# Kernel tuning notes

Hardware: AMD Instinct MI355X
Metric: run time of the kernel (lower is better)

Reference implementation:

```python
import jax, jax.numpy as jnp
import numpy as np

N = 50000
E = 400000
H1, H2, D = 4, 2, 64
NEG_SLOPE = 0.2
EPS = 1e-5


def _segment_softmax(alpha, dst, num_nodes):
    # alpha: [E, H], softmax over edges sharing the same dst node
    m = jax.ops.segment_max(alpha, dst, num_segments=num_nodes)  # [N, H]
    ex = jnp.exp(alpha - m[dst])
    den = jax.ops.segment_sum(ex, dst, num_segments=num_nodes)   # [N, H]
    return ex / den[dst]


def _gat_conv(x, src, dst, eattr, W, We, a_src, a_dst, a_edge, b, heads, num_nodes):
    # x: [N, Fin] -> h: [N, H, D]; eattr: [E, Fe] -> e: [E, H, D]
    h = (x @ W).reshape(num_nodes, heads, D)
    e = (eattr @ We).reshape(-1, heads, D)
    al_src = jnp.einsum('nhd,hd->nh', h, a_src)   # [N, H]
    al_dst = jnp.einsum('nhd,hd->nh', h, a_dst)   # [N, H]
    al_e = jnp.einsum('ehd,hd->eh', e, a_edge)    # [E, H]
    alpha = al_src[src] + al_dst[dst] + al_e
    alpha = jax.nn.leaky_relu(alpha, NEG_SLOPE)
    alpha = _segment_softmax(alpha, dst, num_nodes)
    msg = h[src] * alpha[:, :, None]              # [E, H, D]
    out = jax.ops.segment_sum(msg, dst, num_segments=num_nodes)
    return out.reshape(num_nodes, heads * D) + b


def _graph_norm(x, w, b, mean_scale):
    # PyG GraphNorm over the whole (single) graph
    mean = jnp.mean(x, axis=0, keepdims=True)
    out = x - mean * mean_scale
    var = jnp.mean(out * out, axis=0, keepdims=True)
    return w * out / jnp.sqrt(var + EPS) + b


def _forward(x, edge_index, edge_attr,
             W1, We1, as1, ad1, ae1, b1, gn1_w, gn1_b, gn1_ms,
             W2, We2, as2, ad2, ae2, b2, gn2_w, gn2_b, gn2_ms,
             Wc, bc):
    # add self loops (PyG default), self-loop edge_attr = mean of edge_attr
    loops = jnp.arange(N)
    src = jnp.concatenate([edge_index[0], loops])
    dst = jnp.concatenate([edge_index[1], loops])
    ea_mean = jnp.mean(edge_attr, axis=0, keepdims=True)
    eattr = jnp.concatenate([edge_attr, jnp.broadcast_to(ea_mean, (N, edge_attr.shape[1]))])

    h = _gat_conv(x, src, dst, eattr, W1, We1, as1, ad1, ae1, b1, H1, N)
    h = jax.nn.elu(_graph_norm(h, gn1_w, gn1_b, gn1_ms))
    h = _gat_conv(h, src, dst, eattr, W2, We2, as2, ad2, ae2, b2, H2, N)
    h = jax.nn.elu(_graph_norm(h, gn2_w, gn2_b, gn2_ms))
    return h @ Wc + bc


def setup_inputs() -> dict:
    key = jax.random.key(0)
    ks = jax.random.split(key, 20)
    g = lambda k, shape, fan: jax.random.normal(k, shape, jnp.float32) * (1.0 / np.sqrt(fan))
    inp = {
        'x': jax.random.normal(ks[0], (N, 3), jnp.float32),
        'edge_index': jax.random.randint(ks[1], (2, E), 0, N),
        'edge_attr': jax.random.uniform(ks[2], (E, 2), jnp.float32),
        'W1': g(ks[3], (3, H1 * D), 3),
        'We1': g(ks[4], (2, H1 * D), 2),
        'as1': g(ks[5], (H1, D), D),
        'ad1': g(ks[6], (H1, D), D),
        'ae1': g(ks[7], (H1, D), D),
        'b1': jnp.zeros((H1 * D,), jnp.float32),
        'gn1_w': jnp.ones((H1 * D,), jnp.float32),
        'gn1_b': jnp.zeros((H1 * D,), jnp.float32),
        'gn1_ms': jnp.ones((H1 * D,), jnp.float32),
        'W2': g(ks[8], (H1 * D, H2 * D), H1 * D),
        'We2': g(ks[9], (2, H2 * D), 2),
        'as2': g(ks[10], (H2, D), D),
        'ad2': g(ks[11], (H2, D), D),
        'ae2': g(ks[12], (H2, D), D),
        'b2': jnp.zeros((H2 * D,), jnp.float32),
        'gn2_w': jnp.ones((H2 * D,), jnp.float32),
        'gn2_b': jnp.zeros((H2 * D,), jnp.float32),
        'gn2_ms': jnp.ones((H2 * D,), jnp.float32),
        # classifier 128 -> 13
        'Wc': g(ks[13], (H2 * D, 13), H2 * D),
        'bc': jnp.zeros((13,), jnp.float32),
    }
    return inp


def reference(x, edge_index, edge_attr,
              W1, We1, as1, ad1, ae1, b1, gn1_w, gn1_b, gn1_ms,
              W2, We2, as2, ad2, ae2, b2, gn2_w, gn2_b, gn2_ms,
              Wc, bc):
    return _forward(x, edge_index, edge_attr,
                    W1, We1, as1, ad1, ae1, b1, gn1_w, gn1_b, gn1_ms,
                    W2, We2, as2, ad2, ae2, b2, gn2_w, gn2_b, gn2_ms,
                    Wc, bc)
```

## Files before the change

### kernel.cpp

```cpp
#include <hip/hip_runtime.h>
#include <math.h>

#define NEG_SLOPE 0.2f
#define GEPS 1e-5f

typedef __attribute__((ext_vector_type(8))) short short8;
typedef __attribute__((ext_vector_type(4))) float floatx4;

__device__ __forceinline__ float wave_reduce_sum(float v) {
#pragma unroll
    for (int o = 32; o > 0; o >>= 1) v += __shfl_down(v, o);
    return v;
}

__device__ __forceinline__ ushort f2bf(float f) {
    union { float f; unsigned int i; } c;
    c.f = f;
    unsigned int b = c.i;
    b += 0x7fffu + ((b >> 16) & 1u);
    return (ushort)(b >> 16);
}

__device__ __forceinline__ float bf2f(ushort u) {
    union { unsigned int i; float f; } c;
    c.i = (unsigned int)u << 16;
    return c.f;
}

__device__ __forceinline__ float2 unpack_bf2(unsigned int u) {
    union { unsigned int i; float f; } a, b;
    a.i = u << 16;
    b.i = u & 0xffff0000u;
    return make_float2(a.f, b.f);
}

__device__ __forceinline__ unsigned int pack_bf2(float lo, float hi) {
    return (unsigned int)f2bf(lo) | ((unsigned int)f2bf(hi) << 16);
}

__device__ __forceinline__ float lrelu(float v) {
    return (v > 0.f) ? v : v * NEG_SLOPE;
}

__device__ __forceinline__ float elu_fast(float v) {
    return (v > 0.f) ? v : (__expf(v) - 1.f);
}

__global__ __launch_bounds__(256) void k_pre(
    const float* __restrict__ x, const float* __restrict__ W1,
    const float* __restrict__ as1, const float* __restrict__ ad1,
    const float* __restrict__ ea, const int* __restrict__ dst,
    const float* __restrict__ W2, const float* __restrict__ We1,
    const float* __restrict__ ae1, const float* __restrict__ We2,
    const float* __restrict__ ae2,
    ushort* __restrict__ h1, float* __restrict__ al_s, float* __restrict__ al_d,
    float* __restrict__ ea_sum, int* __restrict__ deg, uint4* __restrict__ Bfrag,
    float* __restrict__ C1, float* __restrict__ C2, int N, int E, int NB1) {
    int b = blockIdx.x;
    if (b < NB1) {
        int u = threadIdx.x >> 7;
        int n = b * 2 + u;
        if (n >= N) return;
        int t = threadIdx.x & 127, lane = threadIdx.x & 63;
        int c0 = 2 * t;
        float x0 = x[3 * n], x1 = x[3 * n + 1], x2 = x[3 * n + 2];
        float h0 = fmaf(x0, W1[c0], fmaf(x1, W1[256 + c0], x2 * W1[512 + c0]));
        float h1v = fmaf(x0, W1[c0 + 1], fmaf(x1, W1[257 + c0], x2 * W1[513 + c0]));
        ((unsigned int*)h1)[(size_t)n * 128 + t] = pack_bf2(h0, h1v);
        float ps = h0 * as1[c0] + h1v * as1[c0 + 1];
        float pd = h0 * ad1[c0] + h1v * ad1[c0 + 1];
#pragma unroll
        for (int o = 16; o > 0; o >>= 1) {
            ps += __shfl_xor(ps, o);
            pd += __shfl_xor(pd, o);
        }
        if ((lane & 31) == 0) {
            int h = c0 >> 6;
            al_s[n * 4 + h] = ps;
            al_d[n * 4 + h] = pd;
        }
        return;
    }
    b -= NB1;
    if (b < 16) {
        int t = b * 256 + threadIdx.x;
        int c = t >> 9, kk = (t >> 6) & 7, L = t & 63;
        int q = L >> 4, n = c * 16 + (L & 15);
        int k0 = kk * 32 + q * 8;
        unsigned int u0 = pack_bf2(W2[(k0 + 0) * 128 + n], W2[(k0 + 1) * 128 + n]);
        unsigned int u1 = pack_bf2(W2[(k0 + 2) * 128 + n], W2[(k0 + 3) * 128 + n]);
        unsigned int u2 = pack_bf2(W2[(k0 + 4) * 128 + n], W2[(k0 + 5) * 128 + n]);
        unsigned int u3 = pack_bf2(W2[(k0 + 6) * 128 + n], W2[(k0 + 7) * 128 + n]);
        Bfrag[t] = make_uint4(u0, u1, u2, u3);
        return;
    }
    if (b == 16) {
        int t = threadIdx.x, h = t >> 6, lane = t & 63;
        float p0 = We1[t] * ae1[t];
        float p1 = We1[256 + t] * ae1[t];
        p0 = wave_reduce_sum(p0);
        p1 = wave_reduce_sum(p1);
        if (lane == 0) { C1[h] = p0; C1[4 + h] = p1; }
        if (t < 128) {
            float q0 = We2[t] * ae2[t];
            float q1 = We2[128 + t] * ae2[t];
            q0 = wave_reduce_sum(q0);
            q1 = wave_reduce_sum(q1);
            if (lane == 0) { C2[h] = q0; C2[2 + h] = q1; }
        }
        return;
    }
    b -= 17;
    const float2* ea2 = (const float2*)ea;
    float s0 = 0.f, s1 = 0.f;
    for (int e = b * 256 + threadIdx.x; e < E; e += 256 * 256) {
        float2 v = ea2[e];
        s0 += v.x; s1 += v.y;
        atomicAdd(&deg[dst[e]], 1);
    }
    s0 = wave_reduce_sum(s0);
    s1 = wave_reduce_sum(s1);
    if ((threadIdx.x & 63) == 0) {
        atomicAdd(&ea_sum[0], s0);
        atomicAdd(&ea_sum[1], s1);
    }
}

__global__ void k_scan1(const int* __restrict__ deg, int* __restrict__ row_ptr,
                        int* __restrict__ bsum, int N) {
    __shared__ int tmp[1024];
    int tid = threadIdx.x;
    int i = blockIdx.x * 1024 + tid;
    int v = (i < N) ? deg[i] : 0;
    tmp[tid] = v;
    __syncthreads();
#pragma unroll
    for (int off = 1; off < 1024; off <<= 1) {
        int t = (tid >= off) ? tmp[tid - off] : 0;
        __syncthreads();
        tmp[tid] += t;
        __syncthreads();
    }
    if (i < N) row_ptr[i + 1] = tmp[tid];
    if (tid == 1023) bsum[blockIdx.x] = tmp[1023];
}

__global__ void k_scan23(int* __restrict__ row_ptr, const int* __restrict__ bsum,
                         const float* __restrict__ ea_sum, const float* __restrict__ C1,
                         const float* __restrict__ C2, float* __restrict__ lE1,
                         float* __restrict__ lE2, int N, int E) {
    __shared__ int off_s;
    int t = threadIdx.x;
    if (blockIdx.x == 0 && t >= 64 && t < 68) {
        int k = t - 64;
        float m0 = ea_sum[0] / (float)E, m1 = ea_sum[1] / (float)E;
        lE1[k] = m0 * C1[k] + m1 * C1[4 + k];
        if (k < 2) lE2[k] = m0 * C2[k] + m1 * C2[2 + k];
    }
    if (t < 64) {
        int v = (t < blockIdx.x) ? bsum[t] : 0;
#pragma unroll
        for (int o = 32; o > 0; o >>= 1) v += __shfl_xor(v, o);
        if (t == 0) off_s = v;
    }
    __syncthreads();
    int off = off_s;
    int i = blockIdx.x * 1024 + t;
    if (i == 0) row_ptr[0] = 0;
    if (i < N) row_ptr[i + 1] += off;
}

__global__ void k_scatfill(const int* __restrict__ dst, const int* __restrict__ src,
                           const float* __restrict__ ea, const int* __restrict__ row_ptr,
                           int* __restrict__ deg, const float* __restrict__ al_s1,
                           const float* __restrict__ al_d1, const float* __restrict__ C1,
                           float4* __restrict__ ed2, uint4* __restrict__ wmp, int E) {
    int e = blockIdx.x * 256 + threadIdx.x;
    if (e >= E) return;
    int d = dst[e];
    int r = atomicSub(&deg[d], 1);
    int slot = row_ptr[d] + r - 1;
    int s = src[e];
    float2 v = ((const float2*)ea)[e];
    float4 as = *(const float4*)(al_s1 + 4 * (size_t)s);
    float4 ad = *(const float4*)(al_d1 + 4 * (size_t)d);
    float w0 = __expf(lrelu(as.x + ad.x + v.x * C1[0] + v.y * C1[4]));
    float w1 = __expf(lrelu(as.y + ad.y + v.x * C1[1] + v.y * C1[5]));
    float w2 = __expf(lrelu(as.z + ad.z + v.x * C1[2] + v.y * C1[6]));
    float w3 = __expf(lrelu(as.w + ad.w + v.x * C1[3] + v.y * C1[7]));
    ed2[slot] = make_float4(__int_as_float(s), __int_as_float(d), v.x, v.y);
    wmp[slot] = make_uint4((unsigned int)s, pack_bf2(w0, w1), pack_bf2(w2, w3), 0u);
}

__global__ void k_fill2(const float4* __restrict__ ed2, const float* __restrict__ al_s2,
                        const float* __restrict__ al_d2, const float* __restrict__ C2,
                        float4* __restrict__ wm2, int E) {
    int e = blockIdx.x * 256 + threadIdx.x;
    if (e >= E) return;
    float4 m = ed2[e];
    int s = __float_as_int(m.x), d = __float_as_int(m.y);
    float2 as = *(const float2*)(al_s2 + 2 * (size_t)s);
    float2 ad = *(const float2*)(al_d2 + 2 * (size_t)d);
    float wA = __expf(lrelu(as.x + ad.x + m.z * C2[0] + m.w * C2[2]));
    float wB = __expf(lrelu(as.y + ad.y + m.z * C2[1] + m.w * C2[3]));
    wm2[e] = make_float4(m.x, wA, wB, 0.f);
}

__global__ __launch_bounds__(256) void k_agg1(const ushort* __restrict__ h1,
                                              const int* __restrict__ row_ptr,
                                              const uint4* __restrict__ wmp,
                                              const float* __restrict__ al_s,
                                              const float* __restrict__ al_d,
                                              const float* __restrict__ lE,
                                              const float* __restrict__ bias,
                                              ushort* __restrict__ out, int N) {
    int n = blockIdx.x * 4 + (threadIdx.x >> 6);
    if (n >= N) return;
    int lane = threadIdx.x & 63;
    int g = lane >> 5, c32 = lane & 31;
    int h = c32 >> 3;
    const uint4* h1u4 = (const uint4*)h1;
    float4 as = *(const float4*)(al_s + 4 * (size_t)n);
    float4 ad = *(const float4*)(al_d + 4 * (size_t)n);
    float4 le = *(const float4*)lE;
    float ws0 = __expf(lrelu(as.x + ad.x + le.x));
    float ws1 = __expf(lrelu(as.y + ad.y + le.y));
    float ws2 = __expf(lrelu(as.z + ad.z + le.z));
    float ws3 = __expf(lrelu(as.w + ad.w + le.w));
    float wsh = (h == 0) ? ws0 : (h == 1) ? ws1 : (h == 2) ? ws2 : ws3;
    uint4 hs = h1u4[(size_t)n * 32 + c32];
    float wself = (g == 0) ? wsh : 0.f;
    float dsum = wself;
    float acc[8];
    {
        float2 t0 = unpack_bf2(hs.x), t1 = unpack_bf2(hs.y);
        float2 t2 = unpack_bf2(hs.z), t3 = unpack_bf2(hs.w);
        acc[0] = wself * t0.x; acc[1] = wself * t0.y;
        acc[2] = wself * t1.x; acc[3] = wself * t1.y;
        acc[4] = wself * t2.x; acc[5] = wself * t2.y;
        acc[6] = wself * t3.x; acc[7] = wself * t3.y;
    }
    int i0 = row_ptr[n];
    int cnt = row_ptr[n + 1] - i0;
    if (cnt > 0) {
        int last = cnt - 1;
        int nit = (cnt + 1) >> 1;
        int j0 = g;     float mkA = 1.f; if (j0 > last) { j0 = last; mkA = 0.f; }
        int j1 = 2 + g; float mkB = 1.f; if (j1 > last) { j1 = last; mkB = 0.f; }
        int j2 = 4 + g; float mkC = 1.f; if (j2 > last) { j2 = last; mkC = 0.f; }
        int j3 = 6 + g; float mkD = 1.f; if (j3 > last) { j3 = last; mkD = 0.f; }
        uint4 meA = wmp[i0 + j0];
        uint4 meB = wmp[i0 + j1];
        uint4 meC = wmp[i0 + j2];
        uint4 meD = wmp[i0 + j3];
        uint4 gvA = h1u4[(size_t)meA.x * 32 + c32];
        uint4 gvB = h1u4[(size_t)meB.x * 32 + c32];
        uint4 gvC = h1u4[(size_t)meC.x * 32 + c32];
        for (int it = 0; it < nit - 1; ++it) {
            uint4 gvD = h1u4[(size_t)meD.x * 32 + c32];
            int jn = 2 * (it + 4) + g;
            float mn = 1.f;
            if (jn > last) { jn = last; mn = 0.f; }
            uint4 meE = wmp[i0 + jn];
            float2 w01 = unpack_bf2(meA.y);
            float2 w23 = unpack_bf2(meA.z);
            float2 wp = (h < 2) ? w01 : w23;
            float wg = ((h & 1) ? wp.y : wp.x) * mkA;
            dsum += wg;
            float2 u;
            u = unpack_bf2(gvA.x); acc[0] = fmaf(wg, u.x, acc[0]); acc[1] = fmaf(wg, u.y, acc[1]);
            u = unpack_bf2(gvA.y); acc[2] = fmaf(wg, u.x, acc[2]); acc[3] = fmaf(wg, u.y, acc[3]);
            u = unpack_bf2(gvA.z); acc[4] = fmaf(wg, u.x, acc[4]); acc[5] = fmaf(wg, u.y, acc[5]);
            u = unpack_bf2(gvA.w); acc[6] = fmaf(wg, u.x, acc[6]); acc[7] = fmaf(wg, u.y, acc[7]);
            meA = meB; meB = meC; meC = meD; meD = meE;
            gvA = gvB; gvB = gvC; gvC = gvD;
            mkA = mkB; mkB = mkC; mkC = mkD; mkD = mn;
        }
        float2 w01 = unpack_bf2(meA.y);
        float2 w23 = unpack_bf2(meA.z);
        float2 wp = (h < 2) ? w01 : w23;
        float wg = ((h & 1) ? wp.y : wp.x) * mkA;
        dsum += wg;
        float2 u;
        u = unpack_bf2(gvA.x); acc[0] = fmaf(wg, u.x, acc[0]); acc[1] = fmaf(wg, u.y, acc[1]);
        u = unpack_bf2(gvA.y); acc[2] = fmaf(wg, u.x, acc[2]); acc[3] = fmaf(wg, u.y, acc[3]);
        u = unpack_bf2(gvA.z); acc[4] = fmaf(wg, u.x, acc[4]); acc[5] = fmaf(wg, u.y, acc[5]);
        u = unpack_bf2(gvA.w); acc[6] = fmaf(wg, u.x, acc[6]); acc[7] = fmaf(wg, u.y, acc[7]);
    }
#pragma unroll
    for (int k = 0; k < 8; ++k) acc[k] += __shfl_xor(acc[k], 32);
    dsum += __shfl_xor(dsum, 32);
    if (g == 0) {
        float inv = 1.f / dsum;
        const float* bp = bias + c32 * 8;
        float4 b0 = *(const float4*)bp;
        float4 b1 = *(const float4*)(bp + 4);
        uint4 o;
        o.x = pack_bf2(fmaf(acc[0], inv, b0.x), fmaf(acc[1], inv, b0.y));
        o.y = pack_bf2(fmaf(acc[2], inv, b0.z), fmaf(acc[3], inv, b0.w));
        o.z = pack_bf2(fmaf(acc[4], inv, b1.x), fmaf(acc[5], inv, b1.y));
        o.w = pack_bf2(fmaf(acc[6], inv, b1.z), fmaf(acc[7], inv, b1.w));
        ((uint4*)out)[(size_t)n * 32 + c32] = o;
    }
}

__global__ __launch_bounds__(256) void k_agg2(const ushort* __restrict__ h2,
                                              const int* __restrict__ row_ptr,
                                              const float4* __restrict__ wm,
                                              const float* __restrict__ al_s,
                                              const float* __restrict__ al_d,
                                              const float* __restrict__ lE,
                                              const float* __restrict__ bias,
                                              ushort* __restrict__ out, int N) {
    int n = blockIdx.x * 4 + (threadIdx.x >> 6);
    if (n >= N) return;
    int lane = threadIdx.x & 63;
    int g = lane >> 4, c16 = lane & 15;
    bool hi = c16 >= 8;
    const uint4* h2u4 = (const uint4*)h2;
    float2 ad = *(const float2*)(al_d + 2 * (size_t)n);
    float2 as = *(const float2*)(al_s + 2 * (size_t)n);
    float wsA = __expf(lrelu(as.x + ad.x + lE[0]));
    float wsB = __expf(lrelu(as.y + ad.y + lE[1]));
    uint4 hs = h2u4[(size_t)n * 16 + c16];
    float wself = (g == 0) ? (hi ? wsB : wsA) : 0.f;
    float dsum = wself;
    float acc[8];
    {
        float2 t0 = unpack_bf2(hs.x), t1 = unpack_bf2(hs.y);
        float2 t2 = unpack_bf2(hs.z), t3 = unpack_bf2(hs.w);
        acc[0] = wself * t0.x; acc[1] = wself * t0.y;
        acc[2] = wself * t1.x; acc[3] = wself * t1.y;
        acc[4] = wself * t2.x; acc[5] = wself * t2.y;
        acc[6] = wself * t3.x; acc[7] = wself * t3.y;
    }
    int i0 = row_ptr[n];
    int cnt = row_ptr[n + 1] - i0;
    if (cnt > 0) {
        int last = cnt - 1;
        int nit = (cnt + 3) >> 2;
        int j0 = g;      float mkA = 1.f; if (j0 > last) { j0 = last; mkA = 0.f; }
        int j1 = 4 + g;  float mkB = 1.f; if (j1 > last) { j1 = last; mkB = 0.f; }
        int j2 = 8 + g;  float mkC = 1.f; if (j2 > last) { j2 = last; mkC = 0.f; }
        int j3 = 12 + g; float mkD = 1.f; if (j3 > last) { j3 = last; mkD = 0.f; }
        float4 meA = wm[i0 + j0];
        float4 meB = wm[i0 + j1];
        float4 meC = wm[i0 + j2];
        float4 meD = wm[i0 + j3];
        uint4 gvA = h2u4[(size_t)__float_as_int(meA.x) * 16 + c16];
        uint4 gvB = h2u4[(size_t)__float_as_int(meB.x) * 16 + c16];
        uint4 gvC = h2u4[(size_t)__float_as_int(meC.x) * 16 + c16];
        for (int it = 0; it < nit - 1; ++it) {
            uint4 gvD = h2u4[(size_t)__float_as_int(meD.x) * 16 + c16];
            int jn = 4 * (it + 4) + g;
            float mn = 1.f;
            if (jn > last) { jn = last; mn = 0.f; }
            float4 meE = wm[i0 + jn];
            float wg = (hi ? meA.z : meA.y) * mkA;
            dsum += wg;
            float2 u;
            u = unpack_bf2(gvA.x); acc[0] = fmaf(wg, u.x, acc[0]); acc[1] = fmaf(wg, u.y, acc[1]);
            u = unpack_bf2(gvA.y); acc[2] = fmaf(wg, u.x, acc[2]); acc[3] = fmaf(wg, u.y, acc[3]);
            u = unpack_bf2(gvA.z); acc[4] = fmaf(wg, u.x, acc[4]); acc[5] = fmaf(wg, u.y, acc[5]);
            u = unpack_bf2(gvA.w); acc[6] = fmaf(wg, u.x, acc[6]); acc[7] = fmaf(wg, u.y, acc[7]);
            meA = meB; meB = meC; meC = meD; meD = meE;
            gvA = gvB; gvB = gvC; gvC = gvD;
            mkA = mkB; mkB = mkC; mkC = mkD; mkD = mn;
        }
        float wg = (hi ? meA.z : meA.y) * mkA;
        dsum += wg;
        float2 u;
        u = unpack_bf2(gvA.x); acc[0] = fmaf(wg, u.x, acc[0]); acc[1] = fmaf(wg, u.y, acc[1]);
        u = unpack_bf2(gvA.y); acc[2] = fmaf(wg, u.x, acc[2]); acc[3] = fmaf(wg, u.y, acc[3]);
        u = unpack_bf2(gvA.z); acc[4] = fmaf(wg, u.x, acc[4]); acc[5] = fmaf(wg, u.y, acc[5]);
        u = unpack_bf2(gvA.w); acc[6] = fmaf(wg, u.x, acc[6]); acc[7] = fmaf(wg, u.y, acc[7]);
    }
#pragma unroll
    for (int k = 0; k < 8; ++k) {
        acc[k] += __shfl_xor(acc[k], 16);
        acc[k] += __shfl_xor(acc[k], 32);
    }
    dsum += __shfl_xor(dsum, 16);
    dsum += __shfl_xor(dsum, 32);
    if (g == 0) {
        float inv = 1.f / dsum;
        const float* bp = bias + c16 * 8;
        float4 b0 = *(const float4*)bp;
        float4 b1 = *(const float4*)(bp + 4);
        uint4 o;
        o.x = pack_bf2(fmaf(acc[0], inv, b0.x), fmaf(acc[1], inv, b0.y));
        o.y = pack_bf2(fmaf(acc[2], inv, b0.z), fmaf(acc[3], inv, b0.w));
        o.z = pack_bf2(fmaf(acc[4], inv, b1.x), fmaf(acc[5], inv, b1.y));
        o.w = pack_bf2(fmaf(acc[6], inv, b1.z), fmaf(acc[7], inv, b1.w));
        ((uint4*)out)[(size_t)n * 16 + c16] = o;
    }
}

template <int C4>
__global__ __launch_bounds__(256) void k_stats_bf(const ushort* __restrict__ x,
                                                  float* __restrict__ stats, int rows) {
    const int C = C4 * 8;
    const int RG = 256 / C4;
    int t = threadIdx.x;
    int c = t & (C4 - 1);
    int rg = t / C4;
    int rpb = (rows + gridDim.x - 1) / gridDim.x;
    int r0 = blockIdx.x * rpb;
    int r1 = r0 + rpb;
    if (r1 > rows) r1 = rows;
    const uint4* xu = (const uint4*)x;
    float s[8] = {0.f, 0.f, 0.f, 0.f, 0.f, 0.f, 0.f, 0.f};
    float q[8] = {0.f, 0.f, 0.f, 0.f, 0.f, 0.f, 0.f, 0.f};
    for (int r = r0 + rg; r < r1; r += RG) {
        uint4 v = xu[(size_t)r * C4 + c];
        float2 a0 = unpack_bf2(v.x), a1 = unpack_bf2(v.y);
        float2 a2 = unpack_bf2(v.z), a3 = unpack_bf2(v.w);
        s[0] += a0.x; q[0] = fmaf(a0.x, a0.x, q[0]);
        s[1] += a0.y; q[1] = fmaf(a0.y, a0.y, q[1]);
        s[2] += a1.x; q[2] = fmaf(a1.x, a1.x, q[2]);
        s[3] += a1.y; q[3] = fmaf(a1.y, a1.y, q[3]);
        s[4] += a2.x; q[4] = fmaf(a2.x, a2.x, q[4]);
        s[5] += a2.y; q[5] = fmaf(a2.y, a2.y, q[5]);
        s[6] += a3.x; q[6] = fmaf(a3.x, a3.x, q[6]);
        s[7] += a3.y; q[7] = fmaf(a3.y, a3.y, q[7]);
    }
    __shared__ float ls[256 * 16];
#pragma unroll
    for (int k = 0; k < 8; ++k) {
        ls[t * 16 + k] = s[k];
        ls[t * 16 + 8 + k] = q[k];
    }
    __syncthreads();
    if (t < C) {
        int cc = t >> 3, k = t & 7;
        float ssum = 0.f, qsum = 0.f;
#pragma unroll
        for (int g = 0; g < RG; ++g) {
            ssum += ls[(g * C4 + cc) * 16 + k];
            qsum += ls[(g * C4 + cc) * 16 + 8 + k];
        }
        atomicAdd(&stats[t], ssum);
        atomicAdd(&stats[C + t], qsum);
    }
}

__global__ __launch_bounds__(256) void k_gemm2_mfma(const ushort* __restrict__ X,
                                                    const float* __restrict__ stats,
                                                    const float* __restrict__ gw,
                                                    const float* __restrict__ gb,
                                                    const float* __restrict__ gms,
                                                    const uint4* __restrict__ Bfrag,
                                                    const float* __restrict__ as2,
                                                    const float* __restrict__ ad2,
                                                    ushort* __restrict__ H2,
                                                    float* __restrict__ al_s,
                                                    float* __restrict__ al_d, int Nn) {
    __shared__ __align__(16) float ABs[512];
    {
        int t = threadIdx.x;
        float inv = 1.f / (float)Nn;
        float mean = stats[t] * inv;
        float cm = mean * gms[t];
        float var = stats[256 + t] * inv - 2.f * cm * mean + cm * cm;
        float A = gw[t] * rsqrtf(var + GEPS);
        ABs[t] = A;
        ABs[256 + t] = gb[t] - A * cm;
    }
    __syncthreads();
    int wave = threadIdx.x >> 6, lane = threadIdx.x & 63;
    int q = lane >> 4, m = lane & 15;
    int rowbase = blockIdx.x * 64 + wave * 16;
    int row = rowbase + m;
    bool valid = row < Nn;
    const uint4* xr4 = (const uint4*)((const unsigned int*)X + (size_t)row * 128);
    uint4 xa[8];
// ... 163 lines not shown
    const float* We2 = (const float*)d_in[13];
    const float* as2 = (const float*)d_in[14];
    const float* ad2 = (const float*)d_in[15];
    const float* ae2 = (const float*)d_in[16];
    const float* b2 = (const float*)d_in[17];
    const float* gn2_w = (const float*)d_in[18];
    const float* gn2_b = (const float*)d_in[19];
    const float* gn2_ms = (const float*)d_in[20];
    const float* Wc = (const float*)d_in[21];
    const float* bc = (const float*)d_in[22];

    const int N = in_sizes[0] / 3;
    const int E = in_sizes[1] / 2;
    const int* srcv = edge_index;
    const int* dstv = edge_index + E;

    char* w = (char*)d_ws;
    auto carveB = [&](size_t bytes) -> void* {
        void* p = (void*)w;
        w += ((bytes + 255) / 256) * 256;
        return p;
    };
    int* deg = (int*)carveB((size_t)N * 4);
    float* ea_sum = (float*)carveB(8);
    float* statsA = (float*)carveB(512 * 4);
    float* statsB = (float*)carveB(256 * 4);
    char* zero_end = w;
    int* row_ptr = (int*)carveB((size_t)(N + 1) * 4);
    int* bsum = (int*)carveB(1024 * 4);
    float4* ed2 = (float4*)carveB((size_t)E * 16);
    uint4* wmp = (uint4*)carveB((size_t)E * 16);
    float4* wm2 = (float4*)wmp;
    float* C1 = (float*)carveB(8 * 4);
    float* lE1 = (float*)carveB(4 * 4);
    float* C2 = (float*)carveB(4 * 4);
    float* lE2 = (float*)carveB(2 * 4);
    uint4* Bfrag = (uint4*)carveB(4096 * 16);
    float* al_s1 = (float*)carveB((size_t)N * 4 * 4);
    float* al_d1 = (float*)carveB((size_t)N * 4 * 4);
    float* al_s2 = (float*)carveB((size_t)N * 2 * 4);
    float* al_d2 = (float*)carveB((size_t)N * 2 * 4);
    ushort* h1b = (ushort*)carveB((size_t)N * 256 * 2);
    ushort* h2b = (ushort*)carveB((size_t)N * 128 * 2);
    ushort* out1b = (ushort*)carveB((size_t)N * 256 * 2);
    ushort* out2b = h1b;

    hipMemsetAsync(deg, 0, (size_t)(zero_end - (char*)deg), stream);

    const int nb1 = (N + 1023) / 1024;
    const int ebl = (E + 255) / 256;
    const int NB1 = (N + 1) / 2;

    k_pre<<<NB1 + 17 + 256, 256, 0, stream>>>(x, W1, as1, ad1, edge_attr, dstv, W2, We1, ae1,
                                              We2, ae2, h1b, al_s1, al_d1, ea_sum, deg, Bfrag,
                                              C1, C2, N, E, NB1);
    k_scan1<<<nb1, 1024, 0, stream>>>(deg, row_ptr, bsum, N);
    k_scan23<<<nb1, 1024, 0, stream>>>(row_ptr, bsum, ea_sum, C1, C2, lE1, lE2, N, E);
    k_scatfill<<<ebl, 256, 0, stream>>>(dstv, srcv, edge_attr, row_ptr, deg, al_s1, al_d1, C1,
                                        ed2, wmp, E);
    k_agg1<<<(N + 3) / 4, 256, 0, stream>>>(h1b, row_ptr, wmp, al_s1, al_d1, lE1, b1, out1b, N);
    k_stats_bf<32><<<256, 256, 0, stream>>>(out1b, statsA, N);
    k_gemm2_mfma<<<(N + 63) / 64, 256, 0, stream>>>(out1b, statsA, gn1_w, gn1_b, gn1_ms, Bfrag,
                                                    as2, ad2, h2b, al_s2, al_d2, N);
    k_fill2<<<ebl, 256, 0, stream>>>(ed2, al_s2, al_d2, C2, wm2, E);
    k_agg2<<<(N + 3) / 4, 256, 0, stream>>>(h2b, row_ptr, wm2, al_s2, al_d2, lE2, b2, out2b, N);
    k_stats_bf<16><<<256, 256, 0, stream>>>(out2b, statsB, N);
    k_cls<<<(N + 15) / 16, 256, 0, stream>>>(out2b, statsB, gn2_w, gn2_b, gn2_ms, Wc, bc,
                                             (float*)d_out, N);
}
```

Measured before the change: 320.9 us.

## Aggregate raw 3-dim inputs before projecting, fuse GraphNorm stats into aggregation

Layer-1 aggregation now uses linearity: it gathers the 3-float source features, accumulates a per-head weighted sum (12 values), and applies W1 after normalisation. This removes the materialised 256-wide bf16 h1 and its heavy per-edge gathers. Attention logits for layer 1 are computed from precomputed W1·a projections inside the scan kernel. Both aggregation kernels become grid-stride and accumulate GraphNorm column sums and squares in place, with block-level atomics replacing the separate stats kernels. The cost is extra shuffle reductions per node and a fixed block count.

```diff
diff --git a/kernel.cpp b/kernel.cpp
--- a/kernel.cpp
+++ b/kernel.cpp
@@ -3,6 +3,8 @@
 
 #define NEG_SLOPE 0.2f
 #define GEPS 1e-5f
+#define AGG1_BLOCKS 2048
+#define AGG2_BLOCKS 2048
 
 typedef __attribute__((ext_vector_type(8))) short short8;
 typedef __attribute__((ext_vector_type(4))) float floatx4;
@@ -47,41 +49,15 @@
 }
 
 __global__ __launch_bounds__(256) void k_pre(
-    const float* __restrict__ x, const float* __restrict__ W1,
-    const float* __restrict__ as1, const float* __restrict__ ad1,
+    const float* __restrict__ W1, const float* __restrict__ as1, const float* __restrict__ ad1,
     const float* __restrict__ ea, const int* __restrict__ dst,
     const float* __restrict__ W2, const float* __restrict__ We1,
     const float* __restrict__ ae1, const float* __restrict__ We2,
     const float* __restrict__ ae2,
-    ushort* __restrict__ h1, float* __restrict__ al_s, float* __restrict__ al_d,
     float* __restrict__ ea_sum, int* __restrict__ deg, uint4* __restrict__ Bfrag,
-    float* __restrict__ C1, float* __restrict__ C2, int N, int E, int NB1) {
+    float* __restrict__ C1, float* __restrict__ C2, float* __restrict__ Ps,
+    float* __restrict__ Pd, int E) {
     int b = blockIdx.x;
-    if (b < NB1) {
-        int u = threadIdx.x >> 7;
-        int n = b * 2 + u;
-        if (n >= N) return;
-        int t = threadIdx.x & 127, lane = threadIdx.x & 63;
-        int c0 = 2 * t;
-        float x0 = x[3 * n], x1 = x[3 * n + 1], x2 = x[3 * n + 2];
-        float h0 = fmaf(x0, W1[c0], fmaf(x1, W1[256 + c0], x2 * W1[512 + c0]));
-        float h1v = fmaf(x0, W1[c0 + 1], fmaf(x1, W1[257 + c0], x2 * W1[513 + c0]));
-        ((unsigned int*)h1)[(size_t)n * 128 + t] = pack_bf2(h0, h1v);
-        float ps = h0 * as1[c0] + h1v * as1[c0 + 1];
-        float pd = h0 * ad1[c0] + h1v * ad1[c0 + 1];
-#pragma unroll
-        for (int o = 16; o > 0; o >>= 1) {
-            ps += __shfl_xor(ps, o);
-            pd += __shfl_xor(pd, o);
-        }
-        if ((lane & 31) == 0) {
-            int h = c0 >> 6;
-            al_s[n * 4 + h] = ps;
-            al_d[n * 4 + h] = pd;
-        }
-        return;
-    }
-    b -= NB1;
     if (b < 16) {
         int t = b * 256 + threadIdx.x;
         int c = t >> 9, kk = (t >> 6) & 7, L = t & 63;
@@ -101,6 +77,14 @@
         p0 = wave_reduce_sum(p0);
         p1 = wave_reduce_sum(p1);
         if (lane == 0) { C1[h] = p0; C1[4 + h] = p1; }
+        float av = as1[t], dv = ad1[t];
+#pragma unroll
+        for (int k = 0; k < 3; ++k) {
+            float wv = W1[k * 256 + t];
+            float ps = wave_reduce_sum(wv * av);
+            float pd = wave_reduce_sum(wv * dv);
+            if (lane == 0) { Ps[h * 3 + k] = ps; Pd[h * 3 + k] = pd; }
+        }
         if (t < 128) {
             float q0 = We2[t] * ae2[t];
             float q1 = We2[128 + t] * ae2[t];
@@ -147,8 +131,10 @@
 
 __global__ void k_scan23(int* __restrict__ row_ptr, const int* __restrict__ bsum,
                          const float* __restrict__ ea_sum, const float* __restrict__ C1,
-                         const float* __restrict__ C2, float* __restrict__ lE1,
-                         float* __restrict__ lE2, int N, int E) {
+                         const float* __restrict__ C2, const float* __restrict__ Ps,
+                         const float* __restrict__ Pd, const float* __restrict__ x,
+                         float* __restrict__ al_s1, float* __restrict__ al_d1,
+                         float* __restrict__ lE1, float* __restrict__ lE2, int N, int E) {
     __shared__ int off_s;
     int t = threadIdx.x;
     if (blockIdx.x == 0 && t >= 64 && t < 68) {
@@ -167,7 +153,21 @@
     int off = off_s;
     int i = blockIdx.x * 1024 + t;
     if (i == 0) row_ptr[0] = 0;
-    if (i < N) row_ptr[i + 1] += off;
+    if (i < N) {
+        row_ptr[i + 1] += off;
+        float x0 = x[3 * i], x1 = x[3 * i + 1], x2 = x[3 * i + 2];
+        float4 sv, dv;
+        sv.x = fmaf(x0, Ps[0], fmaf(x1, Ps[1], x2 * Ps[2]));
+        sv.y = fmaf(x0, Ps[3], fmaf(x1, Ps[4], x2 * Ps[5]));
+        sv.z = fmaf(x0, Ps[6], fmaf(x1, Ps[7], x2 * Ps[8]));
+        sv.w = fmaf(x0, Ps[9], fmaf(x1, Ps[10], x2 * Ps[11]));
+        dv.x = fmaf(x0, Pd[0], fmaf(x1, Pd[1], x2 * Pd[2]));
+        dv.y = fmaf(x0, Pd[3], fmaf(x1, Pd[4], x2 * Pd[5]));
+        dv.z = fmaf(x0, Pd[6], fmaf(x1, Pd[7], x2 * Pd[8]));
+        dv.w = fmaf(x0, Pd[9], fmaf(x1, Pd[10], x2 * Pd[11]));
+        *(float4*)(al_s1 + 4 * (size_t)i) = sv;
+        *(float4*)(al_d1 + 4 * (size_t)i) = dv;
+    }
 }
 
 __global__ void k_scatfill(const int* __restrict__ dst, const int* __restrict__ src,
@@ -206,101 +206,121 @@
     wm2[e] = make_float4(m.x, wA, wB, 0.f);
 }
 
-__global__ __launch_bounds__(256) void k_agg1(const ushort* __restrict__ h1,
+__global__ __launch_bounds__(256) void k_agg1(const float* __restrict__ x,
                                               const int* __restrict__ row_ptr,
                                               const uint4* __restrict__ wmp,
                                               const float* __restrict__ al_s,
                                               const float* __restrict__ al_d,
                                               const float* __restrict__ lE,
+                                              const float* __restrict__ W1,
                                               const float* __restrict__ bias,
-                                              ushort* __restrict__ out, int N) {
-    int n = blockIdx.x * 4 + (threadIdx.x >> 6);
-    if (n >= N) return;
-    int lane = threadIdx.x & 63;
-    int g = lane >> 5, c32 = lane & 31;
-    int h = c32 >> 3;
-    const uint4* h1u4 = (const uint4*)h1;
-    float4 as = *(const float4*)(al_s + 4 * (size_t)n);
-    float4 ad = *(const float4*)(al_d + 4 * (size_t)n);
-    float4 le = *(const float4*)lE;
-    float ws0 = __expf(lrelu(as.x + ad.x + le.x));
-    float ws1 = __expf(lrelu(as.y + ad.y + le.y));
-    float ws2 = __expf(lrelu(as.z + ad.z + le.z));
-    float ws3 = __expf(lrelu(as.w + ad.w + le.w));
-    float wsh = (h == 0) ? ws0 : (h == 1) ? ws1 : (h == 2) ? ws2 : ws3;
-    uint4 hs = h1u4[(size_t)n * 32 + c32];
-    float wself = (g == 0) ? wsh : 0.f;
-    float dsum = wself;
-    float acc[8];
+                                              ushort* __restrict__ out,
+                                              float* __restrict__ stats, int N) {
+    int l = threadIdx.x & 31;
+    int grp = threadIdx.x >> 5;
+    int c0 = l * 8;
+    int hh = l >> 3;
+    float4 wa0 = *(const float4*)(W1 + c0);
+    float4 wa1 = *(const float4*)(W1 + c0 + 4);
+    float4 wb0 = *(const float4*)(W1 + 256 + c0);
+    float4 wb1 = *(const float4*)(W1 + 256 + c0 + 4);
+    float4 wc0 = *(const float4*)(W1 + 512 + c0);
+    float4 wc1 = *(const float4*)(W1 + 512 + c0 + 4);
+    float4 bv0 = *(const float4*)(bias + c0);
+    float4 bv1 = *(const float4*)(bias + c0 + 4);
+    float le0 = lE[0], le1 = lE[1], le2 = lE[2], le3 = lE[3];
+    float s8[8] = {0.f, 0.f, 0.f, 0.f, 0.f, 0.f, 0.f, 0.f};
+    float q8[8] = {0.f, 0.f, 0.f, 0.f, 0.f, 0.f, 0.f, 0.f};
+    for (int n = blockIdx.x * 8 + grp; n < N; n += AGG1_BLOCKS * 8) {
+        float4 asn = *(const float4*)(al_s + 4 * (size_t)n);
+        float4 adn = *(const float4*)(al_d + 4 * (size_t)n);
+        float ws0 = __expf(lrelu(asn.x + adn.x + le0));
+        float ws1 = __expf(lrelu(asn.y + adn.y + le1));
+        float ws2 = __expf(lrelu(asn.z + adn.z + le2));
+        float ws3 = __expf(lrelu(asn.w + adn.w + le3));
+        float z[12];
+        float ds[4];
+#pragma unroll
+        for (int k = 0; k < 12; ++k) z[k] = 0.f;
+#pragma unroll
+        for (int k = 0; k < 4; ++k) ds[k] = 0.f;
+        int i0 = row_ptr[n];
+        int cnt = row_ptr[n + 1] - i0;
+        for (int j = l; j < cnt; j += 32) {
+            uint4 me = wmp[i0 + j];
+            int s = (int)me.x;
+            float xs0 = x[3 * s], xs1 = x[3 * s + 1], xs2 = x[3 * s + 2];
+            float2 w01 = unpack_bf2(me.y);
+            float2 w23 = unpack_bf2(me.z);
+            z[0] = fmaf(w01.x, xs0, z[0]); z[1] = fmaf(w01.x, xs1, z[1]); z[2] = fmaf(w01.x, xs2, z[2]);
+            z[3] = fmaf(w01.y, xs0, z[3]); z[4] = fmaf(w01.y, xs1, z[4]); z[5] = fmaf(w01.y, xs2, z[5]);
+            z[6] = fmaf(w23.x, xs0, z[6]); z[7] = fmaf(w23.x, xs1, z[7]); z[8] = fmaf(w23.x, xs2, z[8]);
+            z[9] = fmaf(w23.y, xs0, z[9]); z[10] = fmaf(w23.y, xs1, z[10]); z[11] = fmaf(w23.y, xs2, z[11]);
+            ds[0] += w01.x; ds[1] += w01.y; ds[2] += w23.x; ds[3] += w23.y;
+        }
+#pragma unroll
+        for (int o = 16; o > 0; o >>= 1) {
+#pragma unroll
+            for (int k = 0; k < 12; ++k) z[k] += __shfl_xor(z[k], o);
+#pragma unroll
+            for (int k = 0; k < 4; ++k) ds[k] += __shfl_xor(ds[k], o);
+        }
+        float xn0 = x[3 * n], xn1 = x[3 * n + 1], xn2 = x[3 * n + 2];
+        z[0] = fmaf(ws0, xn0, z[0]); z[1] = fmaf(ws0, xn1, z[1]); z[2] = fmaf(ws0, xn2, z[2]);
+        z[3] = fmaf(ws1, xn0, z[3]); z[4] = fmaf(ws1, xn1, z[4]); z[5] = fmaf(ws1, xn2, z[5]);
+        z[6] = fmaf(ws2, xn0, z[6]); z[7] = fmaf(ws2, xn1, z[7]); z[8] = fmaf(ws2, xn2, z[8]);
+        z[9] = fmaf(ws3, xn0, z[9]); z[10] = fmaf(ws3, xn1, z[10]); z[11] = fmaf(ws3, xn2, z[11]);
+        ds[0] += ws0; ds[1] += ws1; ds[2] += ws2; ds[3] += ws3;
+        float zh0 = (hh == 0) ? z[0] : (hh == 1) ? z[3] : (hh == 2) ? z[6] : z[9];
+        float zh1 = (hh == 0) ? z[1] : (hh == 1) ? z[4] : (hh == 2) ? z[7] : z[10];
+        float zh2 = (hh == 0) ? z[2] : (hh == 1) ? z[5] : (hh == 2) ? z[8] : z[11];
+        float dsh = (hh == 0) ? ds[0] : (hh == 1) ? ds[1] : (hh == 2) ? ds[2] : ds[3];
+        float inv = 1.f / dsh;
+        float v0 = fmaf(fmaf(zh0, wa0.x, fmaf(zh1, wb0.x, zh2 * wc0.x)), inv, bv0.x);
+        float v1 = fmaf(fmaf(zh0, wa0.y, fmaf(zh1, wb0.y, zh2 * wc0.y)), inv, bv0.y);
+        float v2 = fmaf(fmaf(zh0, wa0.z, fmaf(zh1, wb0.z, zh2 * wc0.z)), inv, bv0.z);
+        float v3 = fmaf(fmaf(zh0, wa0.w, fmaf(zh1, wb0.w, zh2 * wc0.w)), inv, bv0.w);
+        float v4 = fmaf(fmaf(zh0, wa1.x, fmaf(zh1, wb1.x, zh2 * wc1.x)), inv, bv1.x);
+        float v5 = fmaf(fmaf(zh0, wa1.y, fmaf(zh1, wb1.y, zh2 * wc1.y)), inv, bv1.y);
+        float v6 = fmaf(fmaf(zh0, wa1.z, fmaf(zh1, wb1.z, zh2 * wc1.z)), inv, bv1.z);
+        float v7 = fmaf(fmaf(zh0, wa1.w, fmaf(zh1, wb1.w, zh2 * wc1.w)), inv, bv1.w);
+        ushort u0 = f2bf(v0), u1 = f2bf(v1), u2 = f2bf(v2), u3 = f2bf(v3);
+        ushort u4 = f2bf(v4), u5 = f2bf(v5), u6 = f2bf(v6), u7 = f2bf(v7);
+        float r0 = bf2f(u0), r1 = bf2f(u1), r2 = bf2f(u2), r3 = bf2f(u3);
+        float r4 = bf2f(u4), r5 = bf2f(u5), r6 = bf2f(u6), r7 = bf2f(u7);
+        s8[0] += r0; q8[0] = fmaf(r0, r0, q8[0]);
+        s8[1] += r1; q8[1] = fmaf(r1, r1, q8[1]);
+        s8[2] += r2; q8[2] = fmaf(r2, r2, q8[2]);
+        s8[3] += r3; q8[3] = fmaf(r3, r3, q8[3]);
+        s8[4] += r4; q8[4] = fmaf(r4, r4, q8[4]);
+        s8[5] += r5; q8[5] = fmaf(r5, r5, q8[5]);
+        s8[6] += r6; q8[6] = fmaf(r6, r6, q8[6]);
+        s8[7] += r7; q8[7] = fmaf(r7, r7, q8[7]);
+        uint4 o;
+        o.x = (unsigned int)u0 | ((unsigned int)u1 << 16);
+        o.y = (unsigned int)u2 | ((unsigned int)u3 << 16);
+        o.z = (unsigned int)u4 | ((unsigned int)u5 << 16);
+        o.w = (unsigned int)u6 | ((unsigned int)u7 << 16);
+        ((uint4*)out)[(size_t)n * 32 + l] = o;
+    }
+    __shared__ float red[8 * 32 * 16];
+#pragma unroll
+    for (int k = 0; k < 8; ++k) {
+        red[(grp * 32 + l) * 16 + k] = s8[k];
+        red[(grp * 32 + l) * 16 + 8 + k] = q8[k];
+    }
+    __syncthreads();
+    int t = threadIdx.x;
     {
-        float2 t0 = unpack_bf2(hs.x), t1 = unpack_bf2(hs.y);
-        float2 t2 = unpack_bf2(hs.z), t3 = unpack_bf2(hs.w);
-        acc[0] = wself * t0.x; acc[1] = wself * t0.y;
-        acc[2] = wself * t1.x; acc[3] = wself * t1.y;
-        acc[4] = wself * t2.x; acc[5] = wself * t2.y;
-        acc[6] = wself * t3.x; acc[7] = wself * t3.y;
-    }
-    int i0 = row_ptr[n];
-    int cnt = row_ptr[n + 1] - i0;
-    if (cnt > 0) {
-        int last = cnt - 1;
-        int nit = (cnt + 1) >> 1;
-        int j0 = g;     float mkA = 1.f; if (j0 > last) { j0 = last; mkA = 0.f; }
-        int j1 = 2 + g; float mkB = 1.f; if (j1 > last) { j1 = last; mkB = 0.f; }
-        int j2 = 4 + g; float mkC = 1.f; if (j2 > last) { j2 = last; mkC = 0.f; }
-        int j3 = 6 + g; float mkD = 1.f; if (j3 > last) { j3 = last; mkD = 0.f; }
-        uint4 meA = wmp[i0 + j0];
-        uint4 meB = wmp[i0 + j1];
-        uint4 meC = wmp[i0 + j2];
-        uint4 meD = wmp[i0 + j3];
-        uint4 gvA = h1u4[(size_t)meA.x * 32 + c32];
-        uint4 gvB = h1u4[(size_t)meB.x * 32 + c32];
-        uint4 gvC = h1u4[(size_t)meC.x * 32 + c32];
-        for (int it = 0; it < nit - 1; ++it) {
-            uint4 gvD = h1u4[(size_t)meD.x * 32 + c32];
-            int jn = 2 * (it + 4) + g;
-            float mn = 1.f;
-            if (jn > last) { jn = last; mn = 0.f; }
-            uint4 meE = wmp[i0 + jn];
-            float2 w01 = unpack_bf2(meA.y);
-            float2 w23 = unpack_bf2(meA.z);
-            float2 wp = (h < 2) ? w01 : w23;
-            float wg = ((h & 1) ? wp.y : wp.x) * mkA;
-            dsum += wg;
-            float2 u;
-            u = unpack_bf2(gvA.x); acc[0] = fmaf(wg, u.x, acc[0]); acc[1] = fmaf(wg, u.y, acc[1]);
-            u = unpack_bf2(gvA.y); acc[2] = fmaf(wg, u.x, acc[2]); acc[3] = fmaf(wg, u.y, acc[3]);
-            u = unpack_bf2(gvA.z); acc[4] = fmaf(wg, u.x, acc[4]); acc[5] = fmaf(wg, u.y, acc[5]);
-            u = unpack_bf2(gvA.w); acc[6] = fmaf(wg, u.x, acc[6]); acc[7] = fmaf(wg, u.y, acc[7]);
-            meA = meB; meB = meC; meC = meD; meD = meE;
-            gvA = gvB; gvB = gvC; gvC = gvD;
-            mkA = mkB; mkB = mkC; mkC = mkD; mkD = mn;
-        }
-        float2 w01 = unpack_bf2(meA.y);
-        float2 w23 = unpack_bf2(meA.z);
-        float2 wp = (h < 2) ? w01 : w23;
-        float wg = ((h & 1) ? wp.y : wp.x) * mkA;
-        dsum += wg;
-        float2 u;
-        u = unpack_bf2(gvA.x); acc[0] = fmaf(wg, u.x, acc[0]); acc[1] = fmaf(wg, u.y, acc[1]);
-        u = unpack_bf2(gvA.y); acc[2] = fmaf(wg, u.x, acc[2]); acc[3] = fmaf(wg, u.y, acc[3]);
-        u = unpack_bf2(gvA.z); acc[4] = fmaf(wg, u.x, acc[4]); acc[5] = fmaf(wg, u.y, acc[5]);
-        u = unpack_bf2(gvA.w); acc[6] = fmaf(wg, u.x, acc[6]); acc[7] = fmaf(wg, u.y, acc[7]);
-    }
-#pragma unroll
-    for (int k = 0; k < 8; ++k) acc[k] += __shfl_xor(acc[k], 32);
-    dsum += __shfl_xor(dsum, 32);
-    if (g == 0) {
-        float inv = 1.f / dsum;
-        const float* bp = bias + c32 * 8;
-        float4 b0 = *(const float4*)bp;
-        float4 b1 = *(const float4*)(bp + 4);
-        uint4 o;
-        o.x = pack_bf2(fmaf(acc[0], inv, b0.x), fmaf(acc[1], inv, b0.y));
-        o.y = pack_bf2(fmaf(acc[2], inv, b0.z), fmaf(acc[3], inv, b0.w));
-        o.z = pack_bf2(fmaf(acc[4], inv, b1.x), fmaf(acc[5], inv, b1.y));
-        o.w = pack_bf2(fmaf(acc[6], inv, b1.z), fmaf(acc[7], inv, b1.w));
-        ((uint4*)out)[(size_t)n * 32 + c32] = o;
+        int l2 = t >> 3, k = t & 7;
+        float ss = 0.f, qq = 0.f;
+#pragma unroll
+        for (int g = 0; g < 8; ++g) {
+            ss += red[(g * 32 + l2) * 16 + k];
+            qq += red[(g * 32 + l2) * 16 + 8 + k];
+        }
+        atomicAdd(&stats[t], ss);
+        atomicAdd(&stats[256 + t], qq);
     }
 }
 
@@ -311,51 +331,70 @@
                                               const float* __restrict__ al_d,
                                               const float* __restrict__ lE,
                                               const float* __restrict__ bias,
-                                              ushort* __restrict__ out, int N) {
-    int n = blockIdx.x * 4 + (threadIdx.x >> 6);
-    if (n >= N) return;
+                                              ushort* __restrict__ out,
+                                              float* __restrict__ stats, int N) {
     int lane = threadIdx.x & 63;
+    int wv = threadIdx.x >> 6;
     int g = lane >> 4, c16 = lane & 15;
     bool hi = c16 >= 8;
     const uint4* h2u4 = (const uint4*)h2;
-    float2 ad = *(const float2*)(al_d + 2 * (size_t)n);
-    float2 as = *(const float2*)(al_s + 2 * (size_t)n);
-    float wsA = __expf(lrelu(as.x + ad.x + lE[0]));
-    float wsB = __expf(lrelu(as.y + ad.y + lE[1]));
-    uint4 hs = h2u4[(size_t)n * 16 + c16];
-    float wself = (g == 0) ? (hi ? wsB : wsA) : 0.f;
-    float dsum = wself;
-    float acc[8];
-    {
-        float2 t0 = unpack_bf2(hs.x), t1 = unpack_bf2(hs.y);
-        float2 t2 = unpack_bf2(hs.z), t3 = unpack_bf2(hs.w);
-        acc[0] = wself * t0.x; acc[1] = wself * t0.y;
-        acc[2] = wself * t1.x; acc[3] = wself * t1.y;
-        acc[4] = wself * t2.x; acc[5] = wself * t2.y;
-        acc[6] = wself * t3.x; acc[7] = wself * t3.y;
-    }
-    int i0 = row_ptr[n];
-    int cnt = row_ptr[n + 1] - i0;
-    if (cnt > 0) {
-        int last = cnt - 1;
-        int nit = (cnt + 3) >> 2;
-        int j0 = g;      float mkA = 1.f; if (j0 > last) { j0 = last; mkA = 0.f; }
-        int j1 = 4 + g;  float mkB = 1.f; if (j1 > last) { j1 = last; mkB = 0.f; }
-        int j2 = 8 + g;  float mkC = 1.f; if (j2 > last) { j2 = last; mkC = 0.f; }
-        int j3 = 12 + g; float mkD = 1.f; if (j3 > last) { j3 = last; mkD = 0.f; }
-        float4 meA = wm[i0 + j0];
-        float4 meB = wm[i0 + j1];
-        float4 meC = wm[i0 + j2];
-        float4 meD = wm[i0 + j3];
-        uint4 gvA = h2u4[(size_t)__float_as_int(meA.x) * 16 + c16];
-        uint4 gvB = h2u4[(size_t)__float_as_int(meB.x) * 16 + c16];
-        uint4 gvC = h2u4[(size_t)__float_as_int(meC.x) * 16 + c16];
-        for (int it = 0; it < nit - 1; ++it) {
-            uint4 gvD = h2u4[(size_t)__float_as_int(meD.x) * 16 + c16];
-            int jn = 4 * (it + 4) + g;
-            float mn = 1.f;
-            if (jn > last) { jn = last; mn = 0.f; }
-            float4 meE = wm[i0 + jn];
+    float le0 = lE[0], le1 = lE[1];
+    const float* bp = bias + c16 * 8;
+    float4 b0 = *(const float4*)bp;
+    float4 b1 = *(const float4*)(bp + 4);
+    float bb[8] = {b0.x, b0.y, b0.z, b0.w, b1.x, b1.y, b1.z, b1.w};
+    float s8[8] = {0.f, 0.f, 0.f, 0.f, 0.f, 0.f, 0.f, 0.f};
+    float q8[8] = {0.f, 0.f, 0.f, 0.f, 0.f, 0.f, 0.f, 0.f};
+    for (int n = blockIdx.x * 4 + wv; n < N; n += AGG2_BLOCKS * 4) {
+        float2 adn = *(const float2*)(al_d + 2 * (size_t)n);
+        float2 asn = *(const float2*)(al_s + 2 * (size_t)n);
+        float wsA = __expf(lrelu(asn.x + adn.x + le0));
+        float wsB = __expf(lrelu(asn.y + adn.y + le1));
+        uint4 hs = h2u4[(size_t)n * 16 + c16];
+        float wself = (g == 0) ? (hi ? wsB : wsA) : 0.f;
+        float dsum = wself;
+        float acc[8];
+        {
+            float2 t0 = unpack_bf2(hs.x), t1 = unpack_bf2(hs.y);
+            float2 t2 = unpack_bf2(hs.z), t3 = unpack_bf2(hs.w);
+            acc[0] = wself * t0.x; acc[1] = wself * t0.y;
+            acc[2] = wself * t1.x; acc[3] = wself * t1.y;
+            acc[4] = wself * t2.x; acc[5] = wself * t2.y;
+            acc[6] = wself * t3.x; acc[7] = wself * t3.y;
+        }
+        int i0 = row_ptr[n];
+        int cnt = row_ptr[n + 1] - i0;
+        if (cnt > 0) {
+            int last = cnt - 1;
+            int nit = (cnt + 3) >> 2;
+            int j0 = g;      float mkA = 1.f; if (j0 > last) { j0 = last; mkA = 0.f; }
+            int j1 = 4 + g;  float mkB = 1.f; if (j1 > last) { j1 = last; mkB = 0.f; }
+            int j2 = 8 + g;  float mkC = 1.f; if (j2 > last) { j2 = last; mkC = 0.f; }
+            int j3 = 12 + g; float mkD = 1.f; if (j3 > last) { j3 = last; mkD = 0.f; }
+            float4 meA = wm[i0 + j0];
+            float4 meB = wm[i0 + j1];
+            float4 meC = wm[i0 + j2];
+            float4 meD = wm[i0 + j3];
+            uint4 gvA = h2u4[(size_t)__float_as_int(meA.x) * 16 + c16];
+            uint4 gvB = h2u4[(size_t)__float_as_int(meB.x) * 16 + c16];
+            uint4 gvC = h2u4[(size_t)__float_as_int(meC.x) * 16 + c16];
+            for (int it = 0; it < nit - 1; ++it) {
+                uint4 gvD = h2u4[(size_t)__float_as_int(meD.x) * 16 + c16];
+                int jn = 4 * (it + 4) + g;
+                float mn = 1.f;
+                if (jn > last) { jn = last; mn = 0.f; }
+                float4 meE = wm[i0 + jn];
+                float wg = (hi ? meA.z : meA.y) * mkA;
+                dsum += wg;
+                float2 u;
+                u = unpack_bf2(gvA.x); acc[0] = fmaf(wg, u.x, acc[0]); acc[1] = fmaf(wg, u.y, acc[1]);
+                u = unpack_bf2(gvA.y); acc[2] = fmaf(wg, u.x, acc[2]); acc[3] = fmaf(wg, u.y, acc[3]);
+                u = unpack_bf2(gvA.z); acc[4] = fmaf(wg, u.x, acc[4]); acc[5] = fmaf(wg, u.y, acc[5]);
+                u = unpack_bf2(gvA.w); acc[6] = fmaf(wg, u.x, acc[6]); acc[7] = fmaf(wg, u.y, acc[7]);
+                meA = meB; meB = meC; meC = meD; meD = meE;
+                gvA = gvB; gvB = gvC; gvC = gvD;
+                mkA = mkB; mkB = mkC; mkC = mkD; mkD = mn;
+            }
             float wg = (hi ? meA.z : meA.y) * mkA;
             dsum += wg;
             float2 u;
@@ -363,84 +402,49 @@
             u = unpack_bf2(gvA.y); acc[2] = fmaf(wg, u.x, acc[2]); acc[3] = fmaf(wg, u.y, acc[3]);
             u = unpack_bf2(gvA.z); acc[4] = fmaf(wg, u.x, acc[4]); acc[5] = fmaf(wg, u.y, acc[5]);
             u = unpack_bf2(gvA.w); acc[6] = fmaf(wg, u.x, acc[6]); acc[7] = fmaf(wg, u.y, acc[7]);
-            meA = meB; meB = meC; meC = meD; meD = meE;
-            gvA = gvB; gvB = gvC; gvC = gvD;
-            mkA = mkB; mkB = mkC; mkC = mkD; mkD = mn;
-        }
-        float wg = (hi ? meA.z : meA.y) * mkA;
-        dsum += wg;
-        float2 u;
-        u = unpack_bf2(gvA.x); acc[0] = fmaf(wg, u.x, acc[0]); acc[1] = fmaf(wg, u.y, acc[1]);
-        u = unpack_bf2(gvA.y); acc[2] = fmaf(wg, u.x, acc[2]); acc[3] = fmaf(wg, u.y, acc[3]);
-        u = unpack_bf2(gvA.z); acc[4] = fmaf(wg, u.x, acc[4]); acc[5] = fmaf(wg, u.y, acc[5]);
-        u = unpack_bf2(gvA.w); acc[6] = fmaf(wg, u.x, acc[6]); acc[7] = fmaf(wg, u.y, acc[7]);
-    }
-#pragma unroll
-    for (int k = 0; k < 8; ++k) {
-        acc[k] += __shfl_xor(acc[k], 16);
-        acc[k] += __shfl_xor(acc[k], 32);
-    }
-    dsum += __shfl_xor(dsum, 16);
-    dsum += __shfl_xor(dsum, 32);
+        }
+#pragma unroll
+        for (int k = 0; k < 8; ++k) {
+            acc[k] += __shfl_xor(acc[k], 16);
+            acc[k] += __shfl_xor(acc[k], 32);
+        }
+        dsum += __shfl_xor(dsum, 16);
+        dsum += __shfl_xor(dsum, 32);
+        if (g == 0) {
+            float inv = 1.f / dsum;
+            unsigned int ow[4];
+#pragma unroll
+            for (int k = 0; k < 4; ++k) {
+                float va = fmaf(acc[2 * k], inv, bb[2 * k]);
+                float vb = fmaf(acc[2 * k + 1], inv, bb[2 * k + 1]);
+                ushort ua = f2bf(va), ub = f2bf(vb);
+                float ra = bf2f(ua), rb = bf2f(ub);
+                s8[2 * k] += ra;       q8[2 * k] = fmaf(ra, ra, q8[2 * k]);
+                s8[2 * k + 1] += rb;   q8[2 * k + 1] = fmaf(rb, rb, q8[2 * k + 1]);
+                ow[k] = (unsigned int)ua | ((unsigned int)ub << 16);
+            }
+            uint4 o; o.x = ow[0]; o.y = ow[1]; o.z = ow[2]; o.w = ow[3];
+            ((uint4*)out)[(size_t)n * 16 + c16] = o;
+        }
+    }
+    __shared__ float red[4 * 16 * 16];
     if (g == 0) {
-        float inv = 1.f / dsum;
-        const float* bp = bias + c16 * 8;
-        float4 b0 = *(const float4*)bp;
-        float4 b1 = *(const float4*)(bp + 4);
-        uint4 o;
-        o.x = pack_bf2(fmaf(acc[0], inv, b0.x), fmaf(acc[1], inv, b0.y));
-        o.y = pack_bf2(fmaf(acc[2], inv, b0.z), fmaf(acc[3], inv, b0.w));
-        o.z = pack_bf2(fmaf(acc[4], inv, b1.x), fmaf(acc[5], inv, b1.y));
-        o.w = pack_bf2(fmaf(acc[6], inv, b1.z), fmaf(acc[7], inv, b1.w));
-        ((uint4*)out)[(size_t)n * 16 + c16] = o;
-    }
-}
-
-template <int C4>
-__global__ __launch_bounds__(256) void k_stats_bf(const ushort* __restrict__ x,
-                                                  float* __restrict__ stats, int rows) {
-    const int C = C4 * 8;
-    const int RG = 256 / C4;
+#pragma unroll
+        for (int k = 0; k < 8; ++k) {
+            red[(wv * 16 + c16) * 16 + k] = s8[k];
+            red[(wv * 16 + c16) * 16 + 8 + k] = q8[k];
+        }
+    }
+    __syncthreads();
     int t = threadIdx.x;
-    int c = t & (C4 - 1);
-    int rg = t / C4;
-    int rpb = (rows + gridDim.x - 1) / gridDim.x;
-    int r0 = blockIdx.x * rpb;
-    int r1 = r0 + rpb;
-    if (r1 > rows) r1 = rows;
-    const uint4* xu = (const uint4*)x;
-    float s[8] = {0.f, 0.f, 0.f, 0.f, 0.f, 0.f, 0.f, 0.f};
-    float q[8] = {0.f, 0.f, 0.f, 0.f, 0.f, 0.f, 0.f, 0.f};
-    for (int r = r0 + rg; r < r1; r += RG) {
-        uint4 v = xu[(size_t)r * C4 + c];
-        float2 a0 = unpack_bf2(v.x), a1 = unpack_bf2(v.y);
-        float2 a2 = unpack_bf2(v.z), a3 = unpack_bf2(v.w);
-        s[0] += a0.x; q[0] = fmaf(a0.x, a0.x, q[0]);
-        s[1] += a0.y; q[1] = fmaf(a0.y, a0.y, q[1]);
-        s[2] += a1.x; q[2] = fmaf(a1.x, a1.x, q[2]);
-        s[3] += a1.y; q[3] = fmaf(a1.y, a1.y, q[3]);
-        s[4] += a2.x; q[4] = fmaf(a2.x, a2.x, q[4]);
-        s[5] += a2.y; q[5] = fmaf(a2.y, a2.y, q[5]);
-        s[6] += a3.x; q[6] = fmaf(a3.x, a3.x, q[6]);
-        s[7] += a3.y; q[7] = fmaf(a3.y, a3.y, q[7]);
-    }
-    __shared__ float ls[256 * 16];
-#pragma unroll
-    for (int k = 0; k < 8; ++k) {
-        ls[t * 16 + k] = s[k];
-        ls[t * 16 + 8 + k] = q[k];
-    }
-    __syncthreads();
-    if (t < C) {
-        int cc = t >> 3, k = t & 7;
-        float ssum = 0.f, qsum = 0.f;
-#pragma unroll
-        for (int g = 0; g < RG; ++g) {
-            ssum += ls[(g * C4 + cc) * 16 + k];
-            qsum += ls[(g * C4 + cc) * 16 + 8 + k];
-        }
-        atomicAdd(&stats[t], ssum);
-        atomicAdd(&stats[C + t], qsum);
+    if (t < 128) {
+        int cr = t >> 3, k = t & 7;
+        float ss = red[(0 * 16 + cr) * 16 + k] + red[(1 * 16 + cr) * 16 + k] +
+                   red[(2 * 16 + cr) * 16 + k] + red[(3 * 16 + cr) * 16 + k];
+        float qq = red[(0 * 16 + cr) * 16 + 8 + k] + red[(1 * 16 + cr) * 16 + 8 + k] +
+                   red[(2 * 16 + cr) * 16 + 8 + k] + red[(3 * 16 + cr) * 16 + 8 + k];
+        atomicAdd(&stats[t], ss);
+        atomicAdd(&stats[128 + t], qq);
     }
 }
 
@@ -670,39 +674,39 @@
     uint4* wmp = (uint4*)carveB((size_t)E * 16);
     float4* wm2 = (float4*)wmp;
     float* C1 = (float*)carveB(8 * 4);
+    float* C2 = (float*)carveB(4 * 4);
+    float* Ps = (float*)carveB(12 * 4);
+    float* Pd = (float*)carveB(12 * 4);
     float* lE1 = (float*)carveB(4 * 4);
-    float* C2 = (float*)carveB(4 * 4);
     float* lE2 = (float*)carveB(2 * 4);
     uint4* Bfrag = (uint4*)carveB(4096 * 16);
     float* al_s1 = (float*)carveB((size_t)N * 4 * 4);
     float* al_d1 = (float*)carveB((size_t)N * 4 * 4);
     float* al_s2 = (float*)carveB((size_t)N * 2 * 4);
     float* al_d2 = (float*)carveB((size_t)N * 2 * 4);
-    ushort* h1b = (ushort*)carveB((size_t)N * 256 * 2);
     ushort* h2b = (ushort*)carveB((size_t)N * 128 * 2);
     ushort* out1b = (ushort*)carveB((size_t)N * 256 * 2);
-    ushort* out2b = h1b;
+    ushort* out2b = (ushort*)carveB((size_t)N * 128 * 2);
 
     hipMemsetAsync(deg, 0, (size_t)(zero_end - (char*)deg), stream);
 
     const int nb1 = (N + 1023) / 1024;
     const int ebl = (E + 255) / 256;
-    const int NB1 = (N + 1) / 2;
-
-    k_pre<<<NB1 + 17 + 256, 256, 0, stream>>>(x, W1, as1, ad1, edge_attr, dstv, W2, We1, ae1,
-                                              We2, ae2, h1b, al_s1, al_d1, ea_sum, deg, Bfrag,
-                                              C1, C2, N, E, NB1);
+
+    k_pre<<<17 + 256, 256, 0, stream>>>(W1, as1, ad1, edge_attr, dstv, W2, We1, ae1, We2, ae2,
+                                        ea_sum, deg, Bfrag, C1, C2, Ps, Pd, E);
     k_scan1<<<nb1, 1024, 0, stream>>>(deg, row_ptr, bsum, N);
-    k_scan23<<<nb1, 1024, 0, stream>>>(row_ptr, bsum, ea_sum, C1, C2, lE1, lE2, N, E);
+    k_scan23<<<nb1, 1024, 0, stream>>>(row_ptr, bsum, ea_sum, C1, C2, Ps, Pd, x, al_s1, al_d1,
+                                       lE1, lE2, N, E);
     k_scatfill<<<ebl, 256, 0, stream>>>(dstv, srcv, edge_attr, row_ptr, deg, al_s1, al_d1, C1,
                                         ed2, wmp, E);
-    k_agg1<<<(N + 3) / 4, 256, 0, stream>>>(h1b, row_ptr, wmp, al_s1, al_d1, lE1, b1, out1b, N);
-    k_stats_bf<32><<<256, 256, 0, stream>>>(out1b, statsA, N);
+    k_agg1<<<AGG1_BLOCKS, 256, 0, stream>>>(x, row_ptr, wmp, al_s1, al_d1, lE1, W1, b1, out1b,
+                                            statsA, N);
     k_gemm2_mfma<<<(N + 63) / 64, 256, 0, stream>>>(out1b, statsA, gn1_w, gn1_b, gn1_ms, Bfrag,
                                                     as2, ad2, h2b, al_s2, al_d2, N);
     k_fill2<<<ebl, 256, 0, stream>>>(ed2, al_s2, al_d2, C2, wm2, E);
-    k_agg2<<<(N + 3) / 4, 256, 0, stream>>>(h2b, row_ptr, wm2, al_s2, al_d2, lE2, b2, out2b, N);
-    k_stats_bf<16><<<256, 256, 0, stream>>>(out2b, statsB, N);
+    k_agg2<<<AGG2_BLOCKS, 256, 0, stream>>>(h2b, row_ptr, wm2, al_s2, al_d2, lE2, b2, out2b,
+                                            statsB, N);
     k_cls<<<(N + 15) / 16, 256, 0, stream>>>(out2b, statsB, gn2_w, gn2_b, gn2_ms, Wc, bc,
                                              (float*)d_out, N);
 }
```

Result: slower. 347.7 us (+8.3%).
